# Kernel optimization log

Measured on AMD Instinct MI355X. Metric: run time of the kernel, lower is better.

Reference implementation:

```python
import jax, jax.numpy as jnp
import numpy as np

B, H, M, N, D = 8, 8, 512, 512, 64
HID = 16
MIX1 = (1.0 / 2.0) ** 0.5
MIX2 = (1.0 / 16.0) ** 0.5


def setup_inputs() -> dict:
    key = jax.random.key(0)
    ks = jax.random.split(key, 8)
    q = jax.random.normal(ks[0], (B, H, M, D), dtype=jnp.float32)
    k = jax.random.normal(ks[1], (B, H, N, D), dtype=jnp.float32)
    v = jax.random.normal(ks[2], (B, H, N, D), dtype=jnp.float32)
    dmat = jax.random.uniform(ks[3], (B, M, N), dtype=jnp.float32)
    mix_W1 = jax.random.uniform(ks[4], (H, 2, HID), minval=-MIX1, maxval=MIX1, dtype=jnp.float32)
    mix_b1 = jax.random.uniform(ks[5], (H, HID), minval=-MIX1, maxval=MIX1, dtype=jnp.float32)
    mix_W2 = jax.random.uniform(ks[6], (H, HID, 1), minval=-MIX2, maxval=MIX2, dtype=jnp.float32)
    mix_b2 = jax.random.uniform(ks[7], (H, 1), minval=-MIX2, maxval=MIX2, dtype=jnp.float32)
    return {"q": q, "k": k, "v": v, "dmat": dmat,
            "mix_W1": mix_W1, "mix_b1": mix_b1, "mix_W2": mix_W2, "mix_b2": mix_b2}


def reference(q, k, v, dmat, mix_W1, mix_b1, mix_W2, mix_b2):
    # attention scores: [b,h,m,n]
    scale = 1.0 / jnp.sqrt(jnp.float32(k.shape[-1]))
    scores = jnp.einsum("bhmd,bhnd->bhmn", q, k) * scale
    # stack dot-product scores with distance matrix: [b,h,m,n,2]
    mixed = jnp.stack([scores, jnp.broadcast_to(dmat[:, None, :, :], scores.shape)], axis=-1)
    # per-head 2-layer MLP over the 2-channel axis
    h1 = jax.nn.relu(jnp.einsum("bhmnc,hcf->bhmnf", mixed, mix_W1)
                     + mix_b1[None, :, None, None, :])          # [b,h,m,n,HID]
    mixed_scores = (jnp.einsum("bhmnf,hfo->bhmno", h1, mix_W2)[..., 0]
                    + mix_b2[None, :, None, None, 0])            # [b,h,m,n]
    attn = jax.nn.softmax(mixed_scores, axis=-1)
    return jnp.einsum("bhmn,bhnd->bhmd", attn, v)
```

## Files before the change

### kernel.cpp

```cpp
#include <hip/hip_runtime.h>
#include <hip/hip_bf16.h>


typedef __attribute__((ext_vector_type(4))) float f32x4;
typedef __attribute__((ext_vector_type(8))) __bf16 bf16x8;
typedef __attribute__((ext_vector_type(4))) __bf16 bf16x4;

static __device__ __forceinline__ float rlf(float x) {
    return __uint_as_float(__builtin_amdgcn_readfirstlane(__float_as_uint(x)));
}
static __device__ __forceinline__ void cvt2(float x, __bf16& h, __bf16& l) {
    h = (__bf16)x;
    l = (__bf16)(x - (float)h);
}
static __device__ __forceinline__ int sw64(int row, int col) {
    return row * 64 + ((((col >> 3) ^ (row & 7)) << 3) | (col & 7));
}
static __device__ __forceinline__ void dma16(const __bf16* g, __bf16* l) {
    __builtin_amdgcn_global_load_lds(
        (const __attribute__((address_space(1))) unsigned*)g,
        (__attribute__((address_space(3))) unsigned*)l, 16, 0, 0);
}

#define B_ 8
#define H_ 8
#define M_ 512
#define N_ 512
#define D_ 64
#define HID_ 16

__global__ __launch_bounds__(256) void prep_kernel(
    const float* __restrict__ kg, const float* __restrict__ vg,
    __bf16* __restrict__ ws)
{
    __shared__ float vld[64 * 68];
    const int t   = threadIdx.x;
    const int blk = blockIdx.x;
    const long base = (long)blk * 4096;
    __bf16* out = ws + (long)blk * 16384;

#pragma unroll
    for (int it = 0; it < 4; ++it) {
        const int e = it * 1024 + t * 4;
        const int rr = e >> 6, c0 = e & 63;
        f32x4 v4 = *(const f32x4*)(vg + base + e);
        *(f32x4*)(vld + rr * 68 + c0) = v4;
    }

#pragma unroll
    for (int qq = t; qq < 512; qq += 256) {
        const int row = qq >> 3, c = qq & 7;
        const float* src = kg + base + row * 64 + ((c ^ (row & 7)) << 3);
        f32x4 a = *(const f32x4*)src;
        f32x4 b4 = *(const f32x4*)(src + 4);
        bf16x8 hv, lv;
#pragma unroll
        for (int j = 0; j < 4; ++j) {
            __bf16 h, l;
            cvt2(a[j], h, l);  hv[j] = h;     lv[j] = l;
            cvt2(b4[j], h, l); hv[4 + j] = h; lv[4 + j] = l;
        }
        *(bf16x8*)(out + qq * 8) = hv;
        *(bf16x8*)(out + 4096 + qq * 8) = lv;
    }
    __syncthreads();

#pragma unroll
    for (int qq = t; qq < 512; qq += 256) {
        const int d = qq & 63, c = qq >> 6;
        bf16x8 hv, lv;
#pragma unroll
        for (int j = 0; j < 8; ++j) {
            const int n = ((c ^ (d & 7)) << 3) + j;
            __bf16 h, l;
            cvt2(vld[n * 68 + d], h, l);
            hv[j] = h; lv[j] = l;
        }
        const int pos = d * 64 + c * 8;
        *(bf16x8*)(out + 8192 + pos) = hv;
        *(bf16x8*)(out + 12288 + pos) = lv;
    }
}

__global__ __launch_bounds__(256, 2) void msdpa_kernel(
    const float* __restrict__ qg, const __bf16* __restrict__ ws,
    const float* __restrict__ dg, const float* __restrict__ w1g,
    const float* __restrict__ b1g, const float* __restrict__ w2g,
    float* __restrict__ outg)
{
    extern __shared__ __bf16 smem[];
    __bf16* KH  = smem;
    __bf16* KL  = smem + 4096;
    __bf16* VTH = smem + 8192;
    __bf16* VTL = smem + 12288;

    const int tid  = threadIdx.x;
    const int lane = tid & 63;
    const int wv   = tid >> 6;
    const int r16  = lane & 15;
    const int g    = lane >> 4;

    const int bm = blockIdx.x;
    const int h  = blockIdx.y;
    const int b  = blockIdx.z;

    __bf16* PHw = smem + 16384 + wv * 1024;
    __bf16* PLw = smem + 20480 + wv * 1024;

    const float* w1h = w1g + h * 2 * HID_;
    const float* b1h = b1g + h * HID_;
    const float* w2h = w2g + h * HID_;
    float af[HID_], cf[HID_], bf_[HID_], wa[HID_];
    float A = 0.f, C = 0.f, B0 = 0.f;
#pragma unroll
    for (int f = 0; f < HID_; ++f) {
        af[f] = rlf(w1h[f]) * 0.125f;
        cf[f] = rlf(w1h[HID_ + f]);
        bf_[f] = rlf(b1h[f]);
        wa[f] = rlf(w2h[f]) * (1.4426950408889634f * 0.5f);
        A  = fmaf(wa[f], af[f], A);
        C  = fmaf(wa[f], cf[f], C);
        B0 = fmaf(wa[f], bf_[f], B0);
    }

    const long bh = (long)(b * H_ + h);
    const float* qbase = qg + (bh * M_ + (long)bm * 64 + wv * 16 + r16) * D_;
    bf16x8 qh[2], ql[2];
#pragma unroll
    for (int ks = 0; ks < 2; ++ks) {
        f32x4 x0 = *(const f32x4*)(qbase + ks * 32 + g * 8);
        f32x4 x1 = *(const f32x4*)(qbase + ks * 32 + g * 8 + 4);
        bf16x8 hv, lv;
#pragma unroll
        for (int j = 0; j < 4; ++j) {
            __bf16 h_, l_;
            cvt2(x0[j], h_, l_); hv[j] = h_; lv[j] = l_;
            cvt2(x1[j], h_, l_); hv[4 + j] = h_; lv[4 + j] = l_;
        }
        qh[ks] = hv; ql[ks] = lv;
    }

    f32x4 oacc[4];
#pragma unroll
    for (int dt = 0; dt < 4; ++dt) oacc[dt] = f32x4{0.f, 0.f, 0.f, 0.f};
    float mrun = -1e30f, lsum = 0.0f;

    const __bf16* wsbh = ws + bh * (8L * 16384);
    const float* dmp = dg + ((long)b * M_ + (long)bm * 64 + wv * 16 + r16) * N_ + g * 4;

    for (int nt = 0; nt < 8; ++nt) {
        __syncthreads();
        const __bf16* tile = wsbh + nt * 16384;
#pragma unroll
        for (int i = 0; i < 8; ++i)
            dma16(tile + i * 2048 + tid * 8, smem + i * 2048 + tid * 8);
        __syncthreads();

        f32x4 dmv[4];
#pragma unroll
        for (int n16 = 0; n16 < 4; ++n16)
            dmv[n16] = *(const f32x4*)(dmp + nt * 64 + n16 * 16);

        f32x4 sacc[4];
#pragma unroll
        for (int n16 = 0; n16 < 4; ++n16) sacc[n16] = f32x4{0.f, 0.f, 0.f, 0.f};
#pragma unroll
        for (int n16 = 0; n16 < 4; ++n16) {
            const int row = n16 * 16 + r16;
#pragma unroll
            for (int ks = 0; ks < 2; ++ks) {
                const int off = sw64(row, ks * 32 + g * 8);
                bf16x8 kh_ = *(const bf16x8*)(KH + off);
                bf16x8 kl_ = *(const bf16x8*)(KL + off);
                sacc[n16] = __builtin_amdgcn_mfma_f32_16x16x32_bf16(kh_, qh[ks], sacc[n16], 0, 0, 0);
                sacc[n16] = __builtin_amdgcn_mfma_f32_16x16x32_bf16(kh_, ql[ks], sacc[n16], 0, 0, 0);
                sacc[n16] = __builtin_amdgcn_mfma_f32_16x16x32_bf16(kl_, qh[ks], sacc[n16], 0, 0, 0);
            }
        }

        float ms[4][4];
#pragma unroll
        for (int n16 = 0; n16 < 4; ++n16)
#pragma unroll
            for (int r = 0; r < 4; ++r) {
                const float s = sacc[n16][r], d = dmv[n16][r];
                float acc = fmaf(A, s, fmaf(C, d, B0));
#pragma unroll
                for (int f = 0; f < HID_; ++f) {
                    const float u = fmaf(af[f], s, fmaf(cf[f], d, bf_[f]));
                    acc = fmaf(wa[f], fabsf(u), acc);
                }
                ms[n16][r] = acc;
            }

        float mloc = -1e30f;
#pragma unroll
        for (int n16 = 0; n16 < 4; ++n16)
#pragma unroll
            for (int r = 0; r < 4; ++r) mloc = fmaxf(mloc, ms[n16][r]);
        mloc = fmaxf(mloc, __shfl_xor(mloc, 16));
        mloc = fmaxf(mloc, __shfl_xor(mloc, 32));
        const float mnew = fmaxf(mrun, mloc);
        const float sc = exp2f(mrun - mnew);
        mrun = mnew;

        float psum = 0.0f;
#pragma unroll
        for (int n16 = 0; n16 < 4; ++n16) {
            bf16x4 ph4, pl4;
#pragma unroll
            for (int r = 0; r < 4; ++r) {
                const float p = exp2f(ms[n16][r] - mnew);
                psum += p;
                __bf16 h_, l_;
                cvt2(p, h_, l_);
                ph4[r] = h_; pl4[r] = l_;
            }
            const int cc = 2 * n16 + (g >> 1);
            const int pos = r16 * 64 + (((cc ^ (r16 & 7)) << 3) | ((g & 1) << 2));
            *(bf16x4*)(PHw + pos) = ph4;
            *(bf16x4*)(PLw + pos) = pl4;
        }
        lsum = lsum * sc + psum;

        float scm[4];
#pragma unroll
        for (int r = 0; r < 4; ++r) scm[r] = __shfl(sc, g * 4 + r);
#pragma unroll
        for (int dt = 0; dt < 4; ++dt)
#pragma unroll
            for (int r = 0; r < 4; ++r) oacc[dt][r] *= scm[r];

#pragma unroll
        for (int ks = 0; ks < 2; ++ks) {
            const int pofs = r16 * 64 + ((((ks * 4 + g)) ^ (r16 & 7)) << 3);
            bf16x8 pa = *(const bf16x8*)(PHw + pofs);
            bf16x8 pb = *(const bf16x8*)(PLw + pofs);
#pragma unroll
            for (int dt = 0; dt < 4; ++dt) {
                const int vofs = sw64(dt * 16 + r16, ks * 32 + g * 8);
                bf16x8 vh = *(const bf16x8*)(VTH + vofs);
                bf16x8 vl = *(const bf16x8*)(VTL + vofs);
                oacc[dt] = __builtin_amdgcn_mfma_f32_16x16x32_bf16(pa, vh, oacc[dt], 0, 0, 0);
                oacc[dt] = __builtin_amdgcn_mfma_f32_16x16x32_bf16(pa, vl, oacc[dt], 0, 0, 0);
                oacc[dt] = __builtin_amdgcn_mfma_f32_16x16x32_bf16(pb, vh, oacc[dt], 0, 0, 0);
            }
        }
    }

    lsum += __shfl_xor(lsum, 16);
    lsum += __shfl_xor(lsum, 32);
    float linv[4];
#pragma unroll
    for (int r = 0; r < 4; ++r) linv[r] = 1.0f / __shfl(lsum, g * 4 + r);

    float* obase = outg + (bh * M_ + (long)bm * 64 + wv * 16) * D_;
#pragma unroll
    for (int dt = 0; dt < 4; ++dt)
#pragma unroll
        for (int r = 0; r < 4; ++r)
            obase[(g * 4 + r) * D_ + dt * 16 + r16] = oacc[dt][r] * linv[r];
}

extern "C" void kernel_launch(void* const* d_in, const int* in_sizes, int n_in,
                              void* d_out, int out_size, void* d_ws, size_t ws_size,
                              hipStream_t stream) {
    const float* q  = (const float*)d_in[0];
    const float* k  = (const float*)d_in[1];
    const float* v  = (const float*)d_in[2];
    const float* dm = (const float*)d_in[3];
    const float* w1 = (const float*)d_in[4];
    const float* b1 = (const float*)d_in[5];
    const float* w2 = (const float*)d_in[6];
    float* out = (float*)d_out;
    __bf16* ws = (__bf16*)d_ws;

    prep_kernel<<<dim3(512), dim3(256), 0, stream>>>(k, v, ws);

    (void)hipFuncSetAttribute(reinterpret_cast<const void*>(msdpa_kernel),
                              hipFuncAttributeMaxDynamicSharedMemorySize, 65536);
    dim3 grid(M_ / 64, H_, B_);
    msdpa_kernel<<<grid, dim3(256), 49152, stream>>>(q, ws, dm, w1, b1, w2, out);
}
```

Measured before the change: 132.6 us.

## Double-buffer K/V LDS tiles and prefetch dmat rows one tile ahead

Splits LDS into two K/V tile buffers and issues the async global-to-LDS copy for the next tile, plus register loads of the next dmat slice, before computing on the current tile. This removes one barrier per iteration and aims to hide global load latency behind the MFMA and MLP work. Dynamic shared memory grows from 48 KB to 80 KB per block, which could limit residency if two blocks no longer fit per CU. It also adds register pressure from holding the prefetched dmat values.

```diff
diff --git a/kernel.cpp b/kernel.cpp
--- a/kernel.cpp
+++ b/kernel.cpp
@@ -89,10 +89,6 @@
     float* __restrict__ outg)
 {
     extern __shared__ __bf16 smem[];
-    __bf16* KH  = smem;
-    __bf16* KL  = smem + 4096;
-    __bf16* VTH = smem + 8192;
-    __bf16* VTL = smem + 12288;
 
     const int tid  = threadIdx.x;
     const int lane = tid & 63;
@@ -104,8 +100,19 @@
     const int h  = blockIdx.y;
     const int b  = blockIdx.z;
 
-    __bf16* PHw = smem + 16384 + wv * 1024;
-    __bf16* PLw = smem + 20480 + wv * 1024;
+    __bf16* PHw = smem + 32768 + wv * 1024;
+    __bf16* PLw = smem + 36864 + wv * 1024;
+
+    const long bh = (long)(b * H_ + h);
+    const __bf16* wsbh = ws + bh * (8L * 16384);
+    const float* dmp = dg + ((long)b * M_ + (long)bm * 64 + wv * 16 + r16) * N_ + g * 4;
+
+    __bf16* bcur = smem;
+    __bf16* bnxt = smem + 16384;
+
+#pragma unroll
+    for (int i = 0; i < 8; ++i)
+        dma16(wsbh + i * 2048 + tid * 8, bcur + i * 2048 + tid * 8);
 
     const float* w1h = w1g + h * 2 * HID_;
     const float* b1h = b1g + h * HID_;
@@ -123,7 +130,6 @@
         B0 = fmaf(wa[f], bf_[f], B0);
     }
 
-    const long bh = (long)(b * H_ + h);
     const float* qbase = qg + (bh * M_ + (long)bm * 64 + wv * 16 + r16) * D_;
     bf16x8 qh[2], ql[2];
 #pragma unroll
@@ -140,26 +146,33 @@
         qh[ks] = hv; ql[ks] = lv;
     }
 
+    f32x4 dmvc[4], dmvn[4];
+#pragma unroll
+    for (int n16 = 0; n16 < 4; ++n16)
+        dmvc[n16] = *(const f32x4*)(dmp + n16 * 16);
+
     f32x4 oacc[4];
 #pragma unroll
     for (int dt = 0; dt < 4; ++dt) oacc[dt] = f32x4{0.f, 0.f, 0.f, 0.f};
     float mrun = -1e30f, lsum = 0.0f;
 
-    const __bf16* wsbh = ws + bh * (8L * 16384);
-    const float* dmp = dg + ((long)b * M_ + (long)bm * 64 + wv * 16 + r16) * N_ + g * 4;
+    __syncthreads();
 
     for (int nt = 0; nt < 8; ++nt) {
-        __syncthreads();
-        const __bf16* tile = wsbh + nt * 16384;
-#pragma unroll
-        for (int i = 0; i < 8; ++i)
-            dma16(tile + i * 2048 + tid * 8, smem + i * 2048 + tid * 8);
-        __syncthreads();
-
-        f32x4 dmv[4];
-#pragma unroll
-        for (int n16 = 0; n16 < 4; ++n16)
-            dmv[n16] = *(const f32x4*)(dmp + nt * 64 + n16 * 16);
+        if (nt < 7) {
+            const __bf16* tile = wsbh + (nt + 1) * 16384;
+#pragma unroll
+            for (int i = 0; i < 8; ++i)
+                dma16(tile + i * 2048 + tid * 8, bnxt + i * 2048 + tid * 8);
+#pragma unroll
+            for (int n16 = 0; n16 < 4; ++n16)
+                dmvn[n16] = *(const f32x4*)(dmp + (nt + 1) * 64 + n16 * 16);
+        }
+
+        __bf16* KH  = bcur;
+        __bf16* KL  = bcur + 4096;
+        __bf16* VTH = bcur + 8192;
+        __bf16* VTL = bcur + 12288;
 
         f32x4 sacc[4];
 #pragma unroll
@@ -183,7 +196,7 @@
         for (int n16 = 0; n16 < 4; ++n16)
 #pragma unroll
             for (int r = 0; r < 4; ++r) {
-                const float s = sacc[n16][r], d = dmv[n16][r];
+                const float s = sacc[n16][r], d = dmvc[n16][r];
                 float acc = fmaf(A, s, fmaf(C, d, B0));
 #pragma unroll
                 for (int f = 0; f < HID_; ++f) {
@@ -245,6 +258,13 @@
                 oacc[dt] = __builtin_amdgcn_mfma_f32_16x16x32_bf16(pa, vl, oacc[dt], 0, 0, 0);
                 oacc[dt] = __builtin_amdgcn_mfma_f32_16x16x32_bf16(pb, vh, oacc[dt], 0, 0, 0);
             }
+        }
+
+        if (nt < 7) {
+            __syncthreads();
+            __bf16* tmp = bcur; bcur = bnxt; bnxt = tmp;
+#pragma unroll
+            for (int n16 = 0; n16 < 4; ++n16) dmvc[n16] = dmvn[n16];
         }
     }
 
@@ -278,7 +298,7 @@
     prep_kernel<<<dim3(512), dim3(256), 0, stream>>>(k, v, ws);
 
     (void)hipFuncSetAttribute(reinterpret_cast<const void*>(msdpa_kernel),
-                              hipFuncAttributeMaxDynamicSharedMemorySize, 65536);
+                              hipFuncAttributeMaxDynamicSharedMemorySize, 81920);
     dim3 grid(M_ / 64, H_, B_);
-    msdpa_kernel<<<grid, dim3(256), 49152, stream>>>(q, ws, dm, w1, b1, w2, out);
-}
+    msdpa_kernel<<<grid, dim3(256), 81920, stream>>>(q, ws, dm, w1, b1, w2, out);
+}
```

New measurement: 133.2 us. Within noise of the previous version (+0.5%).
